# Performance work log

Hardware: AMD Instinct MI355X
Metric: run time of the kernel (lower is better)

## Reference

```python
import jax, jax.numpy as jnp
import numpy as np

N_NODES = 100000
N_EDGES = 3200000
NODE_DIM = 128
MRI_DIM, COG_DIM, CLIN_DIM, GEN_DIM = 256, 64, 32, 512
N_GRAPHS = 256
N_CLASSES = 3
HID = 16


def setup_inputs() -> dict:
    key = jax.random.key(0)
    ks = jax.random.split(key, 20)
    inp = {
        "x": jax.random.normal(ks[0], (N_NODES, NODE_DIM), jnp.float32),
        "edge_index": jax.random.randint(ks[1], (2, N_EDGES), 0, N_NODES, jnp.int64),
        "batch": jnp.sort(jax.random.randint(ks[2], (N_NODES,), 0, N_GRAPHS, jnp.int64)),
        "mri": jax.random.normal(ks[3], (N_GRAPHS, MRI_DIM), jnp.float32),
        "cog": jax.random.normal(ks[4], (N_GRAPHS, COG_DIM), jnp.float32),
        "clin": jax.random.normal(ks[5], (N_GRAPHS, CLIN_DIM), jnp.float32),
        "genetic": jax.random.normal(ks[6], (N_GRAPHS, GEN_DIM), jnp.float32),
        # GCNConv weight/bias
        "gcn_W": jax.random.normal(ks[7], (NODE_DIM, HID), jnp.float32) / np.sqrt(NODE_DIM),
        "gcn_b": jnp.zeros((HID,), jnp.float32),
        # modality FCs (each -> 4)
        "mri_W": jax.random.normal(ks[8], (MRI_DIM, 4), jnp.float32) / np.sqrt(MRI_DIM),
        "mri_b": jnp.zeros((4,), jnp.float32),
        "cog_W": jax.random.normal(ks[9], (COG_DIM, 4), jnp.float32) / np.sqrt(COG_DIM),
        "cog_b": jnp.zeros((4,), jnp.float32),
        "clin_W": jax.random.normal(ks[10], (CLIN_DIM, 4), jnp.float32) / np.sqrt(CLIN_DIM),
        "clin_b": jnp.zeros((4,), jnp.float32),
        "gen_W": jax.random.normal(ks[11], (GEN_DIM, 4), jnp.float32) / np.sqrt(GEN_DIM),
        "gen_b": jnp.zeros((4,), jnp.float32),
        # classifier: Linear(32,16) -> ReLU -> Dropout(eval: identity) -> Linear(16,3)
        "cls_W1": jax.random.normal(ks[12], (32, HID), jnp.float32) / np.sqrt(32.0),
        "cls_b1": jnp.zeros((HID,), jnp.float32),
        "cls_W2": jax.random.normal(ks[13], (HID, N_CLASSES), jnp.float32) / np.sqrt(HID),
        "cls_b2": jnp.zeros((N_CLASSES,), jnp.float32),
    }
    return inp


def gcn_conv(x, edge_index, W, b):
    # PyG GCNConv: add self-loops, symmetric normalization, scatter-add.
    n = x.shape[0]
    xw = x @ W  # [N, HID]
    loop = jnp.arange(n, dtype=edge_index.dtype)
    src = jnp.concatenate([edge_index[0], loop])
    dst = jnp.concatenate([edge_index[1], loop])
    deg = jax.ops.segment_sum(jnp.ones_like(dst, dtype=xw.dtype), dst, num_segments=n)
    dinv = jnp.where(deg > 0, jax.lax.rsqrt(deg), 0.0)
    norm = dinv[src] * dinv[dst]  # [E+N]
    msg = xw[src] * norm[:, None]  # gather + scale
    out = jax.ops.segment_sum(msg, dst, num_segments=n)  # scatter-add
    return out + b


def global_mean_pool(feat, batch, num_graphs):
    s = jax.ops.segment_sum(feat, batch, num_segments=num_graphs)
    cnt = jax.ops.segment_sum(jnp.ones((feat.shape[0],), feat.dtype), batch, num_segments=num_graphs)
    return s / jnp.maximum(cnt, 1.0)[:, None]


def reference(x, edge_index, batch, mri, cog, clin, genetic,
              gcn_W, gcn_b, mri_W, mri_b, cog_W, cog_b, clin_W, clin_b,
              gen_W, gen_b, cls_W1, cls_b1, cls_W2, cls_b2):
    g = jax.nn.relu(gcn_conv(x, edge_index, gcn_W, gcn_b))  # [N, 16]
    g_emb = global_mean_pool(g, batch, N_GRAPHS)            # [B, 16]
    m = jax.nn.relu(mri @ mri_W + mri_b)
    c = jax.nn.relu(cog @ cog_W + cog_b)
    cl = jax.nn.relu(clin @ clin_W + clin_b)
    ge = jax.nn.relu(genetic @ gen_W + gen_b)
    mm = jnp.concatenate([m, c, cl, ge], axis=1)            # [B, 16]
    comb = jnp.concatenate([g_emb, mm], axis=1)             # [B, 32]
    h = jax.nn.relu(comb @ cls_W1 + cls_b1)                 # dropout is identity in eval
    logits = h @ cls_W2 + cls_b2
    return jax.nn.log_softmax(logits, axis=1)
```

## Files before the change

### kernel.cpp

```cpp
#include <hip/hip_runtime.h>
#include <hip/hip_bf16.h>
#include <math.h>

#define N_NODES   100000
#define N_EDGES   3200000
#define NODE_DIM  128
#define HID       16
#define N_GRAPHS  256

#define BSHIFT    6
#define NPB       64
#define NBUCK     ((N_NODES + NPB - 1) >> BSHIFT)
#define NBLK      256
#define TOT       (NBUCK * NBLK)
#define ACCS      17

#define FIX16  4096.0f
#define IFIX16 (1.0f/4096.0f)
#define FIXP   131072.0f
#define IFIXP  (1.0f/131072.0f)

__device__ __forceinline__ short f2bf(float f) {
    unsigned u = __float_as_uint(f);
    unsigned r = (u + 0x7FFF + ((u >> 16) & 1)) >> 16;
    return (short)r;
}
__device__ __forceinline__ int fx(float v, float s) { return __float2int_rn(v * s); }

typedef __attribute__((ext_vector_type(8))) short bf16x8;
typedef __attribute__((ext_vector_type(4))) float f32x4;
typedef __attribute__((ext_vector_type(4))) int   i32x4;

__global__ __launch_bounds__(1024) void bucket_count(
    const int* __restrict__ dst, int* __restrict__ Mc, int E, int chunk)
{
    __shared__ int cnt[NBUCK];
    const int t = threadIdx.x, b = blockIdx.x;
    for (int k = t; k < NBUCK; k += 1024) cnt[k] = 0;
    __syncthreads();
    int e0 = b * chunk, e1 = min(E, e0 + chunk);
    if (e1 > e0) {
        const int4* d4 = (const int4*)dst;
        for (int i = (e0 >> 2) + t; i < (e1 >> 2); i += 1024) {
            int4 d = d4[i];
            atomicAdd(&cnt[d.x >> BSHIFT], 1);
            atomicAdd(&cnt[d.y >> BSHIFT], 1);
            atomicAdd(&cnt[d.z >> BSHIFT], 1);
            atomicAdd(&cnt[d.w >> BSHIFT], 1);
        }
    }
    __syncthreads();
    for (int k = t; k < NBUCK; k += 1024) Mc[b * NBUCK + k] = cnt[k];
}

__global__ __launch_bounds__(256) void transpose_M(
    const int* __restrict__ A, int* __restrict__ At)
{
    __shared__ int tile[64][65];
    const int kt = blockIdx.x * 64, bt = blockIdx.y * 64;
    const int t = threadIdx.x, tr = t >> 6, tc = t & 63;
    for (int i = tr; i < 64; i += 4) {
        int b = bt + i, k = kt + tc;
        tile[i][tc] = (k < NBUCK) ? A[b * NBUCK + k] : 0;
    }
    __syncthreads();
    for (int i = tr; i < 64; i += 4) {
        int k = kt + i, b = bt + tc;
        if (k < NBUCK) At[k * NBLK + b] = tile[tc][i];
    }
}

__global__ __launch_bounds__(256) void transpose_B(
    const int* __restrict__ A, int* __restrict__ At)
{
    __shared__ int tile[64][65];
    const int bt = blockIdx.x * 64, kt = blockIdx.y * 64;
    const int t = threadIdx.x, tr = t >> 6, tc = t & 63;
    for (int i = tr; i < 64; i += 4) {
        int k = kt + i, b = bt + tc;
        tile[i][tc] = (k < NBUCK) ? A[k * NBLK + b] : 0;
    }
    __syncthreads();
    for (int i = tr; i < 64; i += 4) {
        int b = bt + i, k = kt + tc;
        if (k < NBUCK) At[b * NBUCK + k] = tile[tc][i];
    }
}

__global__ __launch_bounds__(256) void scan_blocksum(
    const int* __restrict__ M, int* __restrict__ bsum, int n)
{
    __shared__ int red[256];
    int t = threadIdx.x;
    int base = blockIdx.x * 2048 + t * 8;
    int s = 0;
    #pragma unroll
    for (int k = 0; k < 8; ++k) { int i = base + k; if (i < n) s += M[i]; }
    red[t] = s; __syncthreads();
    for (int o = 128; o > 0; o >>= 1) {
        if (t < o) red[t] += red[t + o];
        __syncthreads();
    }
    if (t == 0) bsum[blockIdx.x] = red[0];
}

__global__ __launch_bounds__(256) void scan_write2(
    int* __restrict__ M, const int* __restrict__ bsum, int n, int nb)
{
    __shared__ int tmp[256];
    __shared__ int tsum[256];
    int t = threadIdx.x;
    tmp[t] = (t < nb) ? bsum[t] : 0;
    __syncthreads();
    for (int o = 1; o < 256; o <<= 1) {
        int a = (t >= o) ? tmp[t - o] : 0;
        __syncthreads();
        tmp[t] += a;
        __syncthreads();
    }
    const int pre0 = (blockIdx.x > 0) ? tmp[blockIdx.x - 1] : 0;

    int base = blockIdx.x * 2048 + t * 8;
    int v[8]; int s = 0;
    #pragma unroll
    for (int k = 0; k < 8; ++k) { int i = base + k; v[k] = (i < n) ? M[i] : 0; s += v[k]; }
    tsum[t] = s; __syncthreads();
    int mine = s;
    for (int o = 1; o < 256; o <<= 1) {
        int a = (t >= o) ? tsum[t - o] : 0;
        __syncthreads();
        tsum[t] += a;
        __syncthreads();
    }
    int pre = pre0 + tsum[t] - mine;
    #pragma unroll
    for (int k = 0; k < 8; ++k) {
        int i = base + k;
        if (i < n) { M[i] = pre; pre += v[k]; }
    }
}

__global__ __launch_bounds__(1024) void bucket_scatter(
    const int* __restrict__ src, const int* __restrict__ dst,
    const int* __restrict__ srcOff, int* __restrict__ ebuf, int E, int chunk)
{
    __shared__ int cur[NBUCK];
    const int t = threadIdx.x;
    const int b = (blockIdx.x & 7) * (NBLK >> 3) + (blockIdx.x >> 3);
    for (int k = t; k < NBUCK; k += 1024) cur[k] = srcOff[b * NBUCK + k];
    __syncthreads();
    int e0 = b * chunk, e1 = min(E, e0 + chunk);
    if (e1 <= e0) return;
    const i32x4* d4 = (const i32x4*)dst;
    const i32x4* s4 = (const i32x4*)src;
    for (int i = (e0 >> 2) + t; i < (e1 >> 2); i += 1024) {
        i32x4 d = __builtin_nontemporal_load(&d4[i]);
        i32x4 s = __builtin_nontemporal_load(&s4[i]);
        int p;
        p = atomicAdd(&cur[d[0] >> BSHIFT], 1); ebuf[p] = s[0] | ((d[0] & (NPB-1)) << 17);
        p = atomicAdd(&cur[d[1] >> BSHIFT], 1); ebuf[p] = s[1] | ((d[1] & (NPB-1)) << 17);
        p = atomicAdd(&cur[d[2] >> BSHIFT], 1); ebuf[p] = s[2] | ((d[2] & (NPB-1)) << 17);
        p = atomicAdd(&cur[d[3] >> BSHIFT], 1); ebuf[p] = s[3] | ((d[3] & (NPB-1)) << 17);
    }
}

__global__ __launch_bounds__(256) void degxw_kernel(
    const int* __restrict__ offT, const int* __restrict__ ebuf,
    const float* __restrict__ x, const float* __restrict__ W,
    float* __restrict__ dinv, short* __restrict__ xws16, int N, int E)
{
    __shared__ int hist[NPB];
    __shared__ float dloc[NPB];
    const int k = blockIdx.x, t = threadIdx.x;
    const int base = k << BSHIFT;

    if (t < NPB) hist[t] = 0;
    __syncthreads();
    {
        int start = offT[k * NBLK];
        int end = (k == NBUCK - 1) ? E : offT[(k + 1) * NBLK];
        for (int j = start + t; j < end; j += 256)
            atomicAdd(&hist[ebuf[j] >> 17], 1);
    }
    __syncthreads();
    if (t < NPB) {
        float dv = rsqrtf((float)(hist[t] + 1));
        dloc[t] = dv;
        if (base + t < N) dinv[base + t] = dv;
    }
    __syncthreads();

    const int lane = t & 63;
    const int q = lane >> 4, n = lane & 15;
    const int tile_base = base + (t >> 6) * 16;
    if (tile_base >= N) return;

    bf16x8 bfrag[4];
    #pragma unroll
    for (int i = 0; i < 4; ++i)
        #pragma unroll
        for (int j = 0; j < 8; ++j)
            bfrag[i][j] = f2bf(W[(i * 32 + q * 8 + j) * HID + n]);

    const float4* x4 = (const float4*)x;
    const int node = tile_base + n;
    f32x4 d = {0.f, 0.f, 0.f, 0.f};
    #pragma unroll
    for (int i = 0; i < 4; ++i) {
        float4 u0 = make_float4(0.f, 0.f, 0.f, 0.f), u1 = u0;
        if (node < N) {
            u0 = x4[(size_t)node * 32 + i * 8 + q * 2];
            u1 = x4[(size_t)node * 32 + i * 8 + q * 2 + 1];
        }
        bf16x8 a;
        a[0] = f2bf(u0.x); a[1] = f2bf(u0.y); a[2] = f2bf(u0.z); a[3] = f2bf(u0.w);
        a[4] = f2bf(u1.x); a[5] = f2bf(u1.y); a[6] = f2bf(u1.z); a[7] = f2bf(u1.w);
        d = __builtin_amdgcn_mfma_f32_16x16x32_bf16(a, bfrag[i], d, 0, 0, 0);
    }
    #pragma unroll
    for (int r = 0; r < 4; ++r) {
        int nd = tile_base + q * 4 + r;
        if (nd < N) {
            float val = d[r] * dloc[nd - base];
            val = fminf(7.995f, fmaxf(-7.995f, val));
            xws16[(size_t)nd * HID + n] = (short)__float2int_rn(val * FIX16);
        }
    }
}

__global__ __launch_bounds__(256, 8) void gather_pool(
    const int* __restrict__ offT, const int* __restrict__ ebuf,
    const float* __restrict__ dinv, const short* __restrict__ xws16,
    const float* __restrict__ gcn_b, const int* __restrict__ batch,
    int* __restrict__ pool, int* __restrict__ cnt, int N, int E)
{
    __shared__ int acc[NPB * ACCS];
    __shared__ int lpool[16 * HID];
    __shared__ int lcnt[16];
    const int k = blockIdx.x, t = threadIdx.x;
    const int base = k << BSHIFT;

    for (int i = t; i < NPB * ACCS; i += 256) acc[i] = 0;
    lpool[t] = 0;
    if (t < 16) lcnt[t] = 0;

    const int start = offT[k * NBLK];
    const int end = (k == NBUCK - 1) ? E : offT[(k + 1) * NBLK];
    const int Ek = end - start;
    __syncthreads();

    const int sub = t >> 1, h = t & 1;
    const int4* xw4 = (const int4*)xws16;
    const int* eb = ebuf + start;

    int e = sub;
    for (; e + 7 * 128 < Ek; e += 1024) {
        int w[8]; int4 vv[8];
        #pragma unroll
        for (int u = 0; u < 8; ++u) w[u] = eb[e + u * 128];
        #pragma unroll
        for (int u = 0; u < 8; ++u) vv[u] = xw4[(size_t)(w[u] & 0x1FFFF) * 2 + h];
        #pragma unroll
        for (int u = 0; u < 8; ++u) {
            int* p = &acc[(w[u] >> 17) * ACCS + h * 8];
            atomicAdd(p + 0, (vv[u].x << 16) >> 16); atomicAdd(p + 1, vv[u].x >> 16);
            atomicAdd(p + 2, (vv[u].y << 16) >> 16); atomicAdd(p + 3, vv[u].y >> 16);
            atomicAdd(p + 4, (vv[u].z << 16) >> 16); atomicAdd(p + 5, vv[u].z >> 16);
            atomicAdd(p + 6, (vv[u].w << 16) >> 16); atomicAdd(p + 7, vv[u].w >> 16);
        }
    }
    for (; e < Ek; e += 128) {
        int w = eb[e];
        int4 vv = xw4[(size_t)(w & 0x1FFFF) * 2 + h];
        int* p = &acc[(w >> 17) * ACCS + h * 8];
        atomicAdd(p + 0, (vv.x << 16) >> 16); atomicAdd(p + 1, vv.x >> 16);
        atomicAdd(p + 2, (vv.y << 16) >> 16); atomicAdd(p + 3, vv.y >> 16);
        atomicAdd(p + 4, (vv.z << 16) >> 16); atomicAdd(p + 5, vv.z >> 16);
        atomicAdd(p + 6, (vv.w << 16) >> 16); atomicAdd(p + 7, vv.w >> 16);
    }
    __syncthreads();

    int nN = min(NPB, N - base);
    int gmin = batch[base], gmax = batch[base + nN - 1];
    int range = gmax - gmin + 1;
    bool useL = (range <= 16);
    const int sub16 = t >> 4, lane16 = t & 15;
    float bb = gcn_b[lane16];

    for (int i = sub16; i < nN; i += 16) {
        int n = base + i;
        int tot = acc[i * ACCS + lane16] + (int)xws16[(size_t)n * HID + lane16];
        float a = (float)tot * IFIX16;
        float r = fmaxf(fmaf(dinv[n], a, bb), 0.f);
        int g = batch[n];
        int ri = fx(r, FIXP);
        if (useL) {
            atomicAdd(&lpool[(g - gmin) * HID + lane16], ri);
            if (lane16 == 0) atomicAdd(&lcnt[g - gmin], 1);
        } else {
            atomicAdd(&pool[g * HID + lane16], ri);
            if (lane16 == 0) atomicAdd(&cnt[g], 1);
        }
    }
    __syncthreads();

    if (useL) {
        for (int i = t; i < range * HID; i += 256) {
            int vv = lpool[i];
            if (vv != 0) atomicAdd(&pool[gmin * HID + i], vv);
        }
        for (int i = t; i < range; i += 256) {
            int c = lcnt[i];
            if (c != 0) atomicAdd(&cnt[gmin + i], c);
        }
    }
}

__global__ __launch_bounds__(64) void head_kernel(
    const int* __restrict__ pool, const int* __restrict__ cnt,
    const float* __restrict__ mri,  const float* __restrict__ cog,
    const float* __restrict__ clin, const float* __restrict__ gen,
    const float* __restrict__ mriW, const float* __restrict__ mrib,
    const float* __restrict__ cogW, const float* __restrict__ cogb,
    const float* __restrict__ clinW, const float* __restrict__ clinb,
    const float* __restrict__ genW, const float* __restrict__ genb,
    const float* __restrict__ W1, const float* __restrict__ b1,
    const float* __restrict__ W2, const float* __restrict__ b2,
    float* __restrict__ out)
{
    const int g = blockIdx.x;
    const int lane = threadIdx.x;
    __shared__ float comb[32];
    __shared__ float h[HID];

    if (lane < HID) {
        float c = fmaxf((float)cnt[g], 1.f);
        comb[lane] = ((float)pool[g * HID + lane] * IFIXP) / c;
    }

    struct Mod { const float* in; const float* W; const float* b; int K; int off; };
    Mod mods[4] = {
        { mri  + (size_t)g * 256, mriW,  mrib,  256, 16 },
        { cog  + (size_t)g * 64,  cogW,  cogb,  64,  20 },
        { clin + (size_t)g * 32,  clinW, clinb, 32,  24 },
        { gen  + (size_t)g * 512, genW,  genb,  512, 28 },
    };
    for (int m = 0; m < 4; ++m) {
        float p0 = 0.f, p1 = 0.f, p2 = 0.f, p3 = 0.f;
        const float* in = mods[m].in;
        const float* Wm = mods[m].W;
        for (int kk = lane; kk < mods[m].K; kk += 64) {
            float xv = in[kk];
            p0 += xv * Wm[kk * 4 + 0];
            p1 += xv * Wm[kk * 4 + 1];
            p2 += xv * Wm[kk * 4 + 2];
            p3 += xv * Wm[kk * 4 + 3];
        }
        #pragma unroll
        for (int o = 32; o > 0; o >>= 1) {
            p0 += __shfl_down(p0, o);
            p1 += __shfl_down(p1, o);
            p2 += __shfl_down(p2, o);
            p3 += __shfl_down(p3, o);
        }
        if (lane == 0) {
            const float* bm = mods[m].b;
            int o = mods[m].off;
            comb[o + 0] = fmaxf(p0 + bm[0], 0.f);
            comb[o + 1] = fmaxf(p1 + bm[1], 0.f);
            comb[o + 2] = fmaxf(p2 + bm[2], 0.f);
            comb[o + 3] = fmaxf(p3 + bm[3], 0.f);
        }
    }
    __syncthreads();

    if (lane < HID) {
        float a = b1[lane];
        #pragma unroll
        for (int kk = 0; kk < 32; ++kk) a += comb[kk] * W1[kk * HID + lane];
        h[lane] = fmaxf(a, 0.f);
    }
    __syncthreads();

    if (lane == 0) {
        float l0 = b2[0], l1 = b2[1], l2 = b2[2];
        #pragma unroll
        for (int kk = 0; kk < HID; ++kk) {
            float hv = h[kk];
            l0 += hv * W2[kk * 3 + 0];
            l1 += hv * W2[kk * 3 + 1];
            l2 += hv * W2[kk * 3 + 2];
        }
        float mx = fmaxf(l0, fmaxf(l1, l2));
        float lse = mx + logf(expf(l0 - mx) + expf(l1 - mx) + expf(l2 - mx));
        out[g * 3 + 0] = l0 - lse;
        out[g * 3 + 1] = l1 - lse;
        out[g * 3 + 2] = l2 - lse;
    }
}

extern "C" void kernel_launch(void* const* d_in, const int* in_sizes, int n_in,
                              void* d_out, int out_size, void* d_ws, size_t ws_size,
                              hipStream_t stream)
{
    const float* x     = (const float*)d_in[0];
    const int*   eidx  = (const int*)d_in[1];
    const int*   batch = (const int*)d_in[2];
    const float* mri   = (const float*)d_in[3];
    const float* cog   = (const float*)d_in[4];
    const float* clin  = (const float*)d_in[5];
    const float* gen   = (const float*)d_in[6];
    const float* gcn_W = (const float*)d_in[7];
    const float* gcn_b = (const float*)d_in[8];
    const float* mriW  = (const float*)d_in[9];
    const float* mrib  = (const float*)d_in[10];
    const float* cogW  = (const float*)d_in[11];
    const float* cogb  = (const float*)d_in[12];
    const float* clinW = (const float*)d_in[13];
    const float* clinb = (const float*)d_in[14];
    const float* genW  = (const float*)d_in[15];
    const float* genb  = (const float*)d_in[16];
    const float* W1    = (const float*)d_in[17];
    const float* b1    = (const float*)d_in[18];
    const float* W2    = (const float*)d_in[19];
    const float* b2    = (const float*)d_in[20];
    float* out = (float*)d_out;

    const int N = in_sizes[0] / NODE_DIM;
    const int E = in_sizes[1] / 2;
    const int* src = eidx;
    const int* dst = eidx + E;

    float* ws    = (float*)d_ws;
    short* xws16 = (short*)ws;
    float* dinv  = ws + 800000;
    int*   pool  = (int*)(ws + 900000);
    int*   cnt   = (int*)(ws + 904096);
    int*   Mc    = (int*)(ws + 905000);
    int*   offT  = (int*)(ws + 1306000);
    int*   srcOff= (int*)(ws + 1707000);
    int*   bsum  = (int*)(ws + 2108000);
    int*   ebuf  = (int*)(ws + 2109000);

    const int chunkE = (E + NBLK - 1) / NBLK;
    const int scanNB = (TOT + 2047) / 2048;
    const dim3 tgrid((NBUCK + 63) / 64, NBLK / 64);
    const dim3 tgridB(NBLK / 64, (NBUCK + 63) / 64);

    hipMemsetAsync(pool, 0, (N_GRAPHS * HID + N_GRAPHS) * sizeof(int), stream);

    bucket_count<<<NBLK, 1024, 0, stream>>>(dst, Mc, E, chunkE);
    transpose_M<<<tgrid, 256, 0, stream>>>(Mc, offT);
    scan_blocksum<<<scanNB, 256, 0, stream>>>(offT, bsum, TOT);
    scan_write2<<<scanNB, 256, 0, stream>>>(offT, bsum, TOT, scanNB);
    transpose_B<<<tgridB, 256, 0, stream>>>(offT, srcOff);
    bucket_scatter<<<NBLK, 1024, 0, stream>>>(src, dst, srcOff, ebuf, E, chunkE);
    degxw_kernel<<<NBUCK, 256, 0, stream>>>(offT, ebuf, x, gcn_W, dinv, xws16, N, E);
    gather_pool<<<NBUCK, 256, 0, stream>>>(offT, ebuf, dinv, xws16,
                                           gcn_b, batch, pool, cnt, N, E);
    head_kernel<<<N_GRAPHS, 64, 0, stream>>>(
        pool, cnt, mri, cog, clin, gen,
        mriW, mrib, cogW, cogb, clinW, clinb, genW, genb,
        W1, b1, W2, b2, out);
}
```

Measured before the change: 231.4 us.

## Pack paired 16-bit accumulations into 64-bit LDS atomics and drop transpose_B

The gather accumulator now packs two 16-bit fixed-point channels into one 64-bit LDS word and adds it with a single 64-bit atomic, halving the number of shared-memory atomics per edge. The low half is biased by 0x8000 so it stays non-negative, and that bias is removed later using a per-node degree saved by the degree kernel. The degree histogram is split into four per-wave copies to reduce atomic contention. The transpose_B kernel is removed and bucket_scatter reads the strided offT layout directly, trading one launch for less coalesced offset loads. The packing relies on the biased low-half sum fitting in 32 bits, which holds only while node degrees stay moderate.

```diff
diff --git a/kernel.cpp b/kernel.cpp
--- a/kernel.cpp
+++ b/kernel.cpp
@@ -13,7 +13,7 @@
 #define NBUCK     ((N_NODES + NPB - 1) >> BSHIFT)
 #define NBLK      256
 #define TOT       (NBUCK * NBLK)
-#define ACCS      17
+#define ACC64S    9
 
 #define FIX16  4096.0f
 #define IFIX16 (1.0f/4096.0f)
@@ -26,6 +26,11 @@
     return (short)r;
 }
 __device__ __forceinline__ int fx(float v, float s) { return __float2int_rn(v * s); }
+
+__device__ __forceinline__ unsigned long long packA(int w) {
+    return ((unsigned long long)(unsigned)(w >> 16) << 32)
+         | (unsigned)((w & 0xFFFF) ^ 0x8000);
+}
 
 typedef __attribute__((ext_vector_type(8))) short bf16x8;
 typedef __attribute__((ext_vector_type(4))) float f32x4;
@@ -70,23 +75,6 @@
     }
 }
 
-__global__ __launch_bounds__(256) void transpose_B(
-    const int* __restrict__ A, int* __restrict__ At)
-{
-    __shared__ int tile[64][65];
-    const int bt = blockIdx.x * 64, kt = blockIdx.y * 64;
-    const int t = threadIdx.x, tr = t >> 6, tc = t & 63;
-    for (int i = tr; i < 64; i += 4) {
-        int k = kt + i, b = bt + tc;
-        tile[i][tc] = (k < NBUCK) ? A[k * NBLK + b] : 0;
-    }
-    __syncthreads();
-    for (int i = tr; i < 64; i += 4) {
-        int b = bt + i, k = kt + tc;
-        if (k < NBUCK) At[b * NBUCK + k] = tile[tc][i];
-    }
-}
-
 __global__ __launch_bounds__(256) void scan_blocksum(
     const int* __restrict__ M, int* __restrict__ bsum, int n)
 {
@@ -142,12 +130,12 @@
 
 __global__ __launch_bounds__(1024) void bucket_scatter(
     const int* __restrict__ src, const int* __restrict__ dst,
-    const int* __restrict__ srcOff, int* __restrict__ ebuf, int E, int chunk)
+    const int* __restrict__ offT, int* __restrict__ ebuf, int E, int chunk)
 {
     __shared__ int cur[NBUCK];
     const int t = threadIdx.x;
     const int b = (blockIdx.x & 7) * (NBLK >> 3) + (blockIdx.x >> 3);
-    for (int k = t; k < NBUCK; k += 1024) cur[k] = srcOff[b * NBUCK + k];
+    for (int k = t; k < NBUCK; k += 1024) cur[k] = offT[k * NBLK + b];
     __syncthreads();
     int e0 = b * chunk, e1 = min(E, e0 + chunk);
     if (e1 <= e0) return;
@@ -167,26 +155,32 @@
 __global__ __launch_bounds__(256) void degxw_kernel(
     const int* __restrict__ offT, const int* __restrict__ ebuf,
     const float* __restrict__ x, const float* __restrict__ W,
-    float* __restrict__ dinv, short* __restrict__ xws16, int N, int E)
-{
-    __shared__ int hist[NPB];
+    float* __restrict__ dinv, int* __restrict__ degA,
+    short* __restrict__ xws16, int N, int E)
+{
+    __shared__ int hist4[4][72];
     __shared__ float dloc[NPB];
     const int k = blockIdx.x, t = threadIdx.x;
     const int base = k << BSHIFT;
-
-    if (t < NPB) hist[t] = 0;
+    const int wave = t >> 6;
+
+    {
+        int* hp = &hist4[0][0];
+        for (int i = t; i < 4 * 72; i += 256) hp[i] = 0;
+    }
     __syncthreads();
     {
         int start = offT[k * NBLK];
         int end = (k == NBUCK - 1) ? E : offT[(k + 1) * NBLK];
         for (int j = start + t; j < end; j += 256)
-            atomicAdd(&hist[ebuf[j] >> 17], 1);
+            atomicAdd(&hist4[wave][ebuf[j] >> 17], 1);
     }
     __syncthreads();
     if (t < NPB) {
-        float dv = rsqrtf((float)(hist[t] + 1));
+        int dd = hist4[0][t] + hist4[1][t] + hist4[2][t] + hist4[3][t];
+        float dv = rsqrtf((float)(dd + 1));
         dloc[t] = dv;
-        if (base + t < N) dinv[base + t] = dv;
+        if (base + t < N) { dinv[base + t] = dv; degA[base + t] = dd; }
     }
     __syncthreads();
 
@@ -230,17 +224,18 @@
 
 __global__ __launch_bounds__(256, 8) void gather_pool(
     const int* __restrict__ offT, const int* __restrict__ ebuf,
-    const float* __restrict__ dinv, const short* __restrict__ xws16,
-    const float* __restrict__ gcn_b, const int* __restrict__ batch,
-    int* __restrict__ pool, int* __restrict__ cnt, int N, int E)
-{
-    __shared__ int acc[NPB * ACCS];
+    const float* __restrict__ dinv, const int* __restrict__ degA,
+    const short* __restrict__ xws16, const float* __restrict__ gcn_b,
+    const int* __restrict__ batch, int* __restrict__ pool,
+    int* __restrict__ cnt, int N, int E)
+{
+    __shared__ unsigned long long acc64[NPB * ACC64S];
     __shared__ int lpool[16 * HID];
     __shared__ int lcnt[16];
     const int k = blockIdx.x, t = threadIdx.x;
     const int base = k << BSHIFT;
 
-    for (int i = t; i < NPB * ACCS; i += 256) acc[i] = 0;
+    for (int i = t; i < NPB * ACC64S; i += 256) acc64[i] = 0ull;
     lpool[t] = 0;
     if (t < 16) lcnt[t] = 0;
 
@@ -262,21 +257,21 @@
         for (int u = 0; u < 8; ++u) vv[u] = xw4[(size_t)(w[u] & 0x1FFFF) * 2 + h];
         #pragma unroll
         for (int u = 0; u < 8; ++u) {
-            int* p = &acc[(w[u] >> 17) * ACCS + h * 8];
-            atomicAdd(p + 0, (vv[u].x << 16) >> 16); atomicAdd(p + 1, vv[u].x >> 16);
-            atomicAdd(p + 2, (vv[u].y << 16) >> 16); atomicAdd(p + 3, vv[u].y >> 16);
-            atomicAdd(p + 4, (vv[u].z << 16) >> 16); atomicAdd(p + 5, vv[u].z >> 16);
-            atomicAdd(p + 6, (vv[u].w << 16) >> 16); atomicAdd(p + 7, vv[u].w >> 16);
+            unsigned long long* p = &acc64[(w[u] >> 17) * ACC64S + h * 4];
+            atomicAdd(p + 0, packA(vv[u].x));
+            atomicAdd(p + 1, packA(vv[u].y));
+            atomicAdd(p + 2, packA(vv[u].z));
+            atomicAdd(p + 3, packA(vv[u].w));
         }
     }
     for (; e < Ek; e += 128) {
         int w = eb[e];
         int4 vv = xw4[(size_t)(w & 0x1FFFF) * 2 + h];
-        int* p = &acc[(w >> 17) * ACCS + h * 8];
-        atomicAdd(p + 0, (vv.x << 16) >> 16); atomicAdd(p + 1, vv.x >> 16);
-        atomicAdd(p + 2, (vv.y << 16) >> 16); atomicAdd(p + 3, vv.y >> 16);
-        atomicAdd(p + 4, (vv.z << 16) >> 16); atomicAdd(p + 5, vv.z >> 16);
-        atomicAdd(p + 6, (vv.w << 16) >> 16); atomicAdd(p + 7, vv.w >> 16);
+        unsigned long long* p = &acc64[(w >> 17) * ACC64S + h * 4];
+        atomicAdd(p + 0, packA(vv.x));
+        atomicAdd(p + 1, packA(vv.y));
+        atomicAdd(p + 2, packA(vv.z));
+        atomicAdd(p + 3, packA(vv.w));
     }
     __syncthreads();
 
@@ -289,7 +284,11 @@
 
     for (int i = sub16; i < nN; i += 16) {
         int n = base + i;
-        int tot = acc[i * ACCS + lane16] + (int)xws16[(size_t)n * HID + lane16];
+        unsigned long long word = acc64[i * ACC64S + (lane16 >> 1)];
+        int s = (lane16 & 1)
+              ? (int)(unsigned)(word >> 32)
+              : (int)(unsigned)(word & 0xFFFFFFFFull) - degA[n] * 32768;
+        int tot = s + (int)xws16[(size_t)n * HID + lane16];
         float a = (float)tot * IFIX16;
         float r = fmaxf(fmaf(dinv[n], a, bb), 0.f);
         int g = batch[n];
@@ -438,14 +437,13 @@
     int*   cnt   = (int*)(ws + 904096);
     int*   Mc    = (int*)(ws + 905000);
     int*   offT  = (int*)(ws + 1306000);
-    int*   srcOff= (int*)(ws + 1707000);
     int*   bsum  = (int*)(ws + 2108000);
     int*   ebuf  = (int*)(ws + 2109000);
+    int*   degA  = (int*)(ws + 5309000);
 
     const int chunkE = (E + NBLK - 1) / NBLK;
     const int scanNB = (TOT + 2047) / 2048;
     const dim3 tgrid((NBUCK + 63) / 64, NBLK / 64);
-    const dim3 tgridB(NBLK / 64, (NBUCK + 63) / 64);
 
     hipMemsetAsync(pool, 0, (N_GRAPHS * HID + N_GRAPHS) * sizeof(int), stream);
 
@@ -453,10 +451,9 @@
     transpose_M<<<tgrid, 256, 0, stream>>>(Mc, offT);
     scan_blocksum<<<scanNB, 256, 0, stream>>>(offT, bsum, TOT);
     scan_write2<<<scanNB, 256, 0, stream>>>(offT, bsum, TOT, scanNB);
-    transpose_B<<<tgridB, 256, 0, stream>>>(offT, srcOff);
-    bucket_scatter<<<NBLK, 1024, 0, stream>>>(src, dst, srcOff, ebuf, E, chunkE);
-    degxw_kernel<<<NBUCK, 256, 0, stream>>>(offT, ebuf, x, gcn_W, dinv, xws16, N, E);
-    gather_pool<<<NBUCK, 256, 0, stream>>>(offT, ebuf, dinv, xws16,
+    bucket_scatter<<<NBLK, 1024, 0, stream>>>(src, dst, offT, ebuf, E, chunkE);
+    degxw_kernel<<<NBUCK, 256, 0, stream>>>(offT, ebuf, x, gcn_W, dinv, degA, xws16, N, E);
+    gather_pool<<<NBUCK, 256, 0, stream>>>(offT, ebuf, dinv, degA, xws16,
                                            gcn_b, batch, pool, cnt, N, E);
     head_kernel<<<N_GRAPHS, 64, 0, stream>>>(
         pool, cnt, mri, cog, clin, gen,
```

Result: faster. 224.2 us (-3.2%).
